# Kernel tuning notes

Hardware: AMD Instinct MI355X
Metric: run time of the kernel (lower is better)

## Reference

```python
import jax, jax.numpy as jnp
import numpy as np

B, S, D, H, DFF = 4, 2048, 1024, 16, 4096
HD = D // H  # head_dim = 64


def rmsnorm(x, scale, eps=1e-6):
    var = jnp.mean(jnp.square(x), axis=-1, keepdims=True)
    return x * jax.lax.rsqrt(var + eps) * scale


def setup_inputs() -> dict:
    key = jax.random.key(0)
    ks = jax.random.split(key, 16)
    s = 1.0 / np.sqrt(D)
    inp = {
        "x": jax.random.normal(ks[0], (B, S, D), jnp.float32),
        "wq": jax.random.normal(ks[1], (D, D), jnp.float32) * s,
        "bq": jnp.zeros((D,), jnp.float32),
        "wk": jax.random.normal(ks[2], (D, D), jnp.float32) * s,
        "bk": jnp.zeros((D,), jnp.float32),
        "wv": jax.random.normal(ks[3], (D, D), jnp.float32) * s,
        "bv": jnp.zeros((D,), jnp.float32),
        "wbeta": jax.random.normal(ks[4], (D, H), jnp.float32) * s,
        "bbeta": jnp.zeros((H,), jnp.float32),
        "wo": jax.random.normal(ks[5], (D, D), jnp.float32) * s,
        "bo": jnp.zeros((D,), jnp.float32),
        "w1": jax.random.normal(ks[6], (D, DFF), jnp.float32) * s,
        "b1": jnp.zeros((DFF,), jnp.float32),
        "w2": jax.random.normal(ks[7], (DFF, D), jnp.float32) * (1.0 / np.sqrt(DFF)),
        "b2": jnp.zeros((D,), jnp.float32),
        "ln1_scale": jnp.ones((D,), jnp.float32),
        "ln2_scale": jnp.ones((D,), jnp.float32),
    }
    return inp


def gdn_attention(x, wq, bq, wk, bk, wv, bv, wbeta, bbeta, wo, bo):
    b, s, _ = x.shape
    q = (x @ wq + bq).reshape(b, s, H, HD)
    k = (x @ wk + bk).reshape(b, s, H, HD)
    v = (x @ wv + bv).reshape(b, s, H, HD)
    k = k / (jnp.linalg.norm(k, axis=-1, keepdims=True) + 1e-6)
    beta = jax.nn.sigmoid(x @ wbeta + bbeta)[..., None]  # (b, s, H, 1)

    # time-major for scan: (s, b, H, ...)
    q = jnp.transpose(q, (1, 0, 2, 3))
    k = jnp.transpose(k, (1, 0, 2, 3))
    v = jnp.transpose(v, (1, 0, 2, 3))
    beta = jnp.transpose(beta, (1, 0, 2, 3))

    def _step(Sm, inputs):
        q_t, k_t, v_t, beta_t = inputs
        Sk = jnp.einsum('bhde,bhe->bhd', Sm, k_t)
        delta = v_t - Sk
        Sm = Sm + beta_t[..., None] * jnp.einsum('bhd,bhe->bhde', delta, k_t)
        o_t = jnp.einsum('bhde,bhe->bhd', Sm, q_t)
        return Sm, o_t

    S0 = jnp.zeros((b, H, HD, HD), x.dtype)
    _, outputs = jax.lax.scan(_step, S0, (q, k, v, beta))
    outputs = jnp.transpose(outputs, (1, 0, 2, 3)).reshape(b, s, D)
    return outputs @ wo + bo


def reference(x, wq, bq, wk, bk, wv, bv, wbeta, bbeta, wo, bo,
              w1, b1, w2, b2, ln1_scale, ln2_scale):
    residual = x
    h = rmsnorm(x, ln1_scale)
    h = gdn_attention(h, wq, bq, wk, bk, wv, bv, wbeta, bbeta, wo, bo)
    x = h + residual
    residual = x
    h = rmsnorm(x, ln2_scale)
    h = jax.nn.gelu(h @ w1 + b1) @ w2 + b2
    return h + residual
```

## Files before the change

### kernel.cpp

```cpp
#include <hip/hip_runtime.h>

#define DEV __device__ __forceinline__

typedef short bf16x8 __attribute__((ext_vector_type(8)));
typedef float f32x4 __attribute__((ext_vector_type(4)));
typedef unsigned int uint;

DEV unsigned short f2b(float f) {
    uint u = __float_as_uint(f);
    u += 0x7fffu + ((u >> 16) & 1u);
    return (unsigned short)(u >> 16);
}
DEV uint packbf2(float a, float b) { return (uint)f2b(a) | ((uint)f2b(b) << 16); }
DEV float b2f(unsigned short s) { return __uint_as_float(((uint)s) << 16); }
DEV float b2f_lo(uint u) { return __uint_as_float(u << 16); }
DEV float b2f_hi(uint u) { return __uint_as_float(u & 0xffff0000u); }

DEV void async_cp16(const void* g, void* l) {
    __builtin_amdgcn_global_load_lds(
        (const __attribute__((address_space(1))) unsigned int*)g,
        (__attribute__((address_space(3))) unsigned int*)l, 16, 0, 0);
}

DEV float quad_sum(float x) {
    x += __int_as_float(__builtin_amdgcn_update_dpp(0, __float_as_int(x), 0xB1, 0xF, 0xF, true));
    x += __int_as_float(__builtin_amdgcn_update_dpp(0, __float_as_int(x), 0x4E, 0xF, 0xF, true));
    return x;
}

DEV float gelu_f(float u) {
    float p = u + 0.044715f * u * u * u;
    float e = __expf(-1.5957691216f * p);
    return __fdividef(u, 1.f + e);
}

DEV void dec8(uint4 p, float* o) {
    o[0] = b2f_lo(p.x); o[1] = b2f_hi(p.x); o[2] = b2f_lo(p.y); o[3] = b2f_hi(p.y);
    o[4] = b2f_lo(p.z); o[5] = b2f_hi(p.z); o[6] = b2f_lo(p.w); o[7] = b2f_hi(p.w);
}

__global__ __launch_bounds__(256) void transpose_cast_k(
    const float* __restrict__ in, unsigned short* __restrict__ out, int K, int N)
{
    __shared__ float tile[32][33];
    const int k0 = blockIdx.x * 32, n0 = blockIdx.y * 32;
    const int tx = threadIdx.x & 31, ty = threadIdx.x >> 5;
#pragma unroll
    for (int i = 0; i < 32; i += 8) {
        int n = n0 + tx;
        tile[ty + i][tx] = (n < N) ? in[(size_t)(k0 + ty + i) * N + n] : 0.0f;
    }
    __syncthreads();
#pragma unroll
    for (int i = 0; i < 32; i += 8) {
        out[(size_t)(n0 + ty + i) * K + (k0 + tx)] = f2b(tile[tx][ty + i]);
    }
}

__global__ void build_bias_k(const float* __restrict__ bq, const float* __restrict__ bk,
                             const float* __restrict__ bv, const float* __restrict__ bb,
                             float* __restrict__ outb)
{
    int i = blockIdx.x * 256 + threadIdx.x;
    if (i >= 3200) return;
    float v = 0.f;
    if (i < 1024)      v = bq[i];
    else if (i < 2048) v = bk[i - 1024];
    else if (i < 3072) v = bv[i - 2048];
    else if (i < 3088) v = bb[i - 3072];
    outb[i] = v;
}

__global__ __launch_bounds__(256) void rmsnorm_cast_k(
    const float* __restrict__ x, const float* __restrict__ scale,
    unsigned short* __restrict__ out)
{
    const int row = blockIdx.x;
    const int t = threadIdx.x;
    const float4 v = *(const float4*)(x + (size_t)row * 1024 + t * 4);
    float ss = v.x * v.x + v.y * v.y + v.z * v.z + v.w * v.w;
#pragma unroll
    for (int off = 1; off < 64; off <<= 1) ss += __shfl_xor(ss, off);
    __shared__ float wsum[4];
    if ((t & 63) == 0) wsum[t >> 6] = ss;
    __syncthreads();
    const float tot = wsum[0] + wsum[1] + wsum[2] + wsum[3];
    const float inv = rsqrtf(tot * (1.0f / 1024.0f) + 1e-6f);
    const float4 sc = *(const float4*)(scale + t * 4);
    uint lo = (uint)f2b(v.x * inv * sc.x) | ((uint)f2b(v.y * inv * sc.y) << 16);
    uint hi = (uint)f2b(v.z * inv * sc.z) | ((uint)f2b(v.w * inv * sc.w) << 16);
    uint2 pkd; pkd.x = lo; pkd.y = hi;
    *(uint2*)(out + (size_t)row * 1024 + t * 4) = pkd;
}

template <int MODE>
__global__ __launch_bounds__(256) void gemm_bt(
    const unsigned short* __restrict__ A, const unsigned short* __restrict__ BT,
    const float* __restrict__ bias, const float* __restrict__ add,
    void* __restrict__ Cout, int N, int K)
{
    __shared__ unsigned short As[128 * 32];
    __shared__ unsigned short Bs[128 * 32];
    const int tid = threadIdx.x;
    const int wid = tid >> 6;
    const int lane = tid & 63;
    const int m0 = blockIdx.x * 128;
    const int n0 = blockIdx.y * 128;

    const int lrow = lane >> 2;
    const int lkw = (((lane & 3) ^ ((lane >> 3) & 3))) * 8;

    const unsigned short* Ag0 = A + (size_t)(m0 + wid * 16 + lrow) * K + lkw;
    const unsigned short* Ag1 = A + (size_t)(m0 + wid * 16 + 64 + lrow) * K + lkw;
    const unsigned short* Bg0 = BT + (size_t)(n0 + wid * 16 + lrow) * K + lkw;
    const unsigned short* Bg1 = BT + (size_t)(n0 + wid * 16 + 64 + lrow) * K + lkw;
    unsigned short* As0 = &As[(wid * 16) * 32];
    unsigned short* As1 = &As[(wid * 16 + 64) * 32];
    unsigned short* Bs0 = &Bs[(wid * 16) * 32];
    unsigned short* Bs1 = &Bs[(wid * 16 + 64) * 32];

    f32x4 acc[4][4];
#pragma unroll
    for (int i = 0; i < 4; i++)
#pragma unroll
        for (int j = 0; j < 4; j++) acc[i][j] = (f32x4)0.f;

    const int wm = (wid & 1) * 64;
    const int wn = (wid >> 1) * 64;
    const int l16 = lane & 15;
    const int quad = lane >> 4;
    const int koffs = (quad ^ ((l16 >> 1) & 3)) * 8;

    for (int k0 = 0; k0 < K; k0 += 32) {
        async_cp16(Ag0 + k0, As0);
        async_cp16(Ag1 + k0, As1);
        async_cp16(Bg0 + k0, Bs0);
        async_cp16(Bg1 + k0, Bs1);
        __syncthreads();
        bf16x8 af[4], bfv[4];
#pragma unroll
        for (int i = 0; i < 4; i++) af[i] = *(const bf16x8*)&As[(wm + i * 16 + l16) * 32 + koffs];
#pragma unroll
        for (int j = 0; j < 4; j++) bfv[j] = *(const bf16x8*)&Bs[(wn + j * 16 + l16) * 32 + koffs];
#pragma unroll
        for (int i = 0; i < 4; i++)
#pragma unroll
            for (int j = 0; j < 4; j++)
                acc[i][j] = __builtin_amdgcn_mfma_f32_16x16x32_bf16(af[i], bfv[j], acc[i][j], 0, 0, 0);
        __syncthreads();
    }

    if (MODE == 2 || MODE == 3) {
        float* ep = ((wid & 2) ? (float*)Bs : (float*)As) + (wid & 1) * 1024;
        const int rr = lane >> 2, cg = lane & 3;
        unsigned short* Cu = (unsigned short*)Cout;
#pragma unroll
        for (int i = 0; i < 4; i++) {
#pragma unroll
            for (int p = 0; p < 2; p++) {
#pragma unroll
                for (int jj = 0; jj < 2; jj++) {
                    const int j = 2 * p + jj;
                    const float bv = bias[n0 + wn + j * 16 + l16];
#pragma unroll
                    for (int r = 0; r < 4; r++) {
                        float v = acc[i][j][r] + bv;
                        if (MODE == 2) v = gelu_f(v);
                        ep[(jj * 16 + l16) * 17 + quad * 4 + r] = v;
                    }
                }
                __syncthreads();
                uint4 pk;
                float f[8];
#pragma unroll
                for (int m = 0; m < 8; m++) f[m] = ep[(cg * 8 + m) * 17 + rr];
                pk.x = packbf2(f[0], f[1]); pk.y = packbf2(f[2], f[3]);
                pk.z = packbf2(f[4], f[5]); pk.w = packbf2(f[6], f[7]);
                *(uint4*)(Cu + (size_t)(m0 + wm + i * 16 + rr) * N + (n0 + wn + p * 32 + cg * 8)) = pk;
                __syncthreads();
            }
        }
    } else {
#pragma unroll
        for (int j = 0; j < 4; j++) {
            const int cg2 = n0 + wn + j * 16 + l16;
            const float bv = bias[cg2];
#pragma unroll
            for (int i = 0; i < 4; i++) {
                const int rg0 = m0 + wm + i * 16 + quad * 4;
#pragma unroll
                for (int r = 0; r < 4; r++) {
                    size_t idx = (size_t)(rg0 + r) * N + cg2;
                    float v = acc[i][j][r] + bv;
                    if (MODE == 1) v += add[idx];
                    ((float*)Cout)[idx] = v;
                }
            }
        }
    }
}


__global__ __launch_bounds__(256) void gdn_prep(
    unsigned short* __restrict__ qkv, unsigned short* __restrict__ Wg,
    unsigned short* __restrict__ ZTg, unsigned short* __restrict__ KTg)
{
    const int chunk = blockIdx.x, bh = blockIdx.y;
    const int b = bh >> 4, h = bh & 15;
    __shared__ float Ks[64 * 68];
    __shared__ float Ws[64 * 65];
    __shared__ float Zs[64 * 65];
    __shared__ float Asl[64 * 65];
    __shared__ float bs[64];
    const int tid = threadIdx.x;
    const int t = tid >> 2, c = tid & 3;
    unsigned short* rowp = qkv + (size_t)(b * 2048 + chunk * 64 + t) * 3200;

    float kn[16];
    {
        uint4 ka = *(const uint4*)(rowp + 1024 + h * 64 + 16 * c);
        uint4 kb = *(const uint4*)(rowp + 1024 + h * 64 + 16 * c + 8);
        dec8(ka, kn); dec8(kb, kn + 8);
    }
    float ss = 0.f;
#pragma unroll
    for (int j = 0; j < 16; j++) ss += kn[j] * kn[j];
    ss = quad_sum(ss);
    const float inv = 1.f / (sqrtf(ss) + 1e-6f);
#pragma unroll
    for (int j = 0; j < 16; j++) kn[j] *= inv;
#pragma unroll
    for (int j = 0; j < 16; j++) Ks[t * 68 + 16 * c + j] = kn[j];
    {
        uint4 p0, p1;
        p0.x = packbf2(kn[0], kn[1]);  p0.y = packbf2(kn[2], kn[3]);
        p0.z = packbf2(kn[4], kn[5]);  p0.w = packbf2(kn[6], kn[7]);
        p1.x = packbf2(kn[8], kn[9]);  p1.y = packbf2(kn[10], kn[11]);
        p1.z = packbf2(kn[12], kn[13]); p1.w = packbf2(kn[14], kn[15]);
        *(uint4*)(rowp + 1024 + h * 64 + 16 * c) = p0;
        *(uint4*)(rowp + 1024 + h * 64 + 16 * c + 8) = p1;
    }
    if (c == 0) bs[t] = 1.f / (1.f + __expf(-b2f(rowp[3072 + h])));
    __syncthreads();

    const float beta = bs[t];
#pragma unroll
    for (int j = 0; j < 16; j++) Ws[t * 65 + 16 * c + j] = beta * kn[j];
    {
        float vv[16];
        uint4 va = *(const uint4*)(rowp + 2048 + h * 64 + 16 * c);
        uint4 vb = *(const uint4*)(rowp + 2048 + h * 64 + 16 * c + 8);
        dec8(va, vv); dec8(vb, vv + 8);
#pragma unroll
        for (int j = 0; j < 16; j++) Zs[t * 65 + 16 * c + j] = beta * vv[j];
    }
    __syncthreads();

    {
        const int tt = tid >> 4, sx = tid & 15;
        float dm[4][4];
#pragma unroll
        for (int i = 0; i < 4; i++)
#pragma unroll
            for (int j = 0; j < 4; j++) dm[i][j] = 0.f;
        for (int d = 0; d < 64; d++) {
            float kt[4], ksv[4];
#pragma unroll
            for (int i = 0; i < 4; i++) kt[i] = Ks[(4 * tt + i) * 68 + d];
#pragma unroll
            for (int j = 0; j < 4; j++) ksv[j] = Ks[(4 * sx + j) * 68 + d];
#pragma unroll
            for (int i = 0; i < 4; i++)
#pragma unroll
                for (int j = 0; j < 4; j++) dm[i][j] += kt[i] * ksv[j];
        }
#pragma unroll
        for (int i = 0; i < 4; i++)
#pragma unroll
            for (int j = 0; j < 4; j++) {
                int T = 4 * tt + i, S_ = 4 * sx + j;
                Asl[T * 65 + S_] = (S_ < T) ? bs[T] * dm[i][j] : 0.f;
            }
    }
    __syncthreads();

    {
        const int wid = tid >> 6, lane = tid & 63;
        for (int qi = 0; qi < 4; qi++) {
            if (qi > 0) {
                const int tb = qi * 16 + wid * 4;
                float aw[4], az[4];
#pragma unroll
                for (int i = 0; i < 4; i++) { aw[i] = Ws[(tb + i) * 65 + lane]; az[i] = Zs[(tb + i) * 65 + lane]; }
                for (int s = 0; s < qi * 16; s++) {
                    float wsv = Ws[s * 65 + lane], zsv = Zs[s * 65 + lane];
#pragma unroll
                    for (int i = 0; i < 4; i++) {
                        float a = Asl[(tb + i) * 65 + s];
                        aw[i] -= a * wsv; az[i] -= a * zsv;
                    }
                }
#pragma unroll
                for (int i = 0; i < 4; i++) { Ws[(tb + i) * 65 + lane] = aw[i]; Zs[(tb + i) * 65 + lane] = az[i]; }
            }
            __syncthreads();
            if (wid == 0) {
                for (int T = qi * 16; T < qi * 16 + 16; T++) {
                    float a_ = Ws[T * 65 + lane];
                    for (int s = qi * 16; s < T; s++) a_ -= Asl[T * 65 + s] * Ws[s * 65 + lane];
                    Ws[T * 65 + lane] = a_;
                }
            } else if (wid == 1) {
                for (int T = qi * 16; T < qi * 16 + 16; T++) {
                    float a_ = Zs[T * 65 + lane];
                    for (int s = qi * 16; s < T; s++) a_ -= Asl[T * 65 + s] * Zs[s * 65 + lane];
                    Zs[T * 65 + lane] = a_;
                }
            }
            __syncthreads();
        }
    }

    const size_t cbase = ((size_t)bh * 32 + chunk) * 4096;
    {
#pragma unroll
        for (int half = 0; half < 2; half++) {
            uint4 w4;
            w4.x = packbf2(Ws[t * 65 + 16 * c + half * 8 + 0], Ws[t * 65 + 16 * c + half * 8 + 1]);
            w4.y = packbf2(Ws[t * 65 + 16 * c + half * 8 + 2], Ws[t * 65 + 16 * c + half * 8 + 3]);
            w4.z = packbf2(Ws[t * 65 + 16 * c + half * 8 + 4], Ws[t * 65 + 16 * c + half * 8 + 5]);
            w4.w = packbf2(Ws[t * 65 + 16 * c + half * 8 + 6], Ws[t * 65 + 16 * c + half * 8 + 7]);
            *(uint4*)(Wg + cbase + (size_t)((2 * c + half) * 64 + t) * 8) = w4;
        }
    }
    {
        const int jj = tid >> 2, tq = tid & 3;
#pragma unroll
        for (int half = 0; half < 2; half++) {
            uint4 z4;
            int i0 = half * 8;
            z4.x = packbf2(Zs[(16 * tq + i0 + 0) * 65 + jj], Zs[(16 * tq + i0 + 1) * 65 + jj]);
            z4.y = packbf2(Zs[(16 * tq + i0 + 2) * 65 + jj], Zs[(16 * tq + i0 + 3) * 65 + jj]);
            z4.z = packbf2(Zs[(16 * tq + i0 + 4) * 65 + jj], Zs[(16 * tq + i0 + 5) * 65 + jj]);
            z4.w = packbf2(Zs[(16 * tq + i0 + 6) * 65 + jj], Zs[(16 * tq + i0 + 7) * 65 + jj]);
            *(uint4*)(ZTg + cbase + (size_t)((2 * tq + half) * 64 + jj) * 8) = z4;
        }
    }
    {
        const int dd = tid >> 2, tq = tid & 3;
#pragma unroll
        for (int half = 0; half < 2; half++) {
            uint4 k4;
            int i0 = half * 8;
            k4.x = packbf2(Ks[(16 * tq + i0 + 0) * 68 + dd], Ks[(16 * tq + i0 + 1) * 68 + dd]);
            k4.y = packbf2(Ks[(16 * tq + i0 + 2) * 68 + dd], Ks[(16 * tq + i0 + 3) * 68 + dd]);
            k4.z = packbf2(Ks[(16 * tq + i0 + 4) * 68 + dd], Ks[(16 * tq + i0 + 5) * 68 + dd]);
            k4.w = packbf2(Ks[(16 * tq + i0 + 6) * 68 + dd], Ks[(16 * tq + i0 + 7) * 68 + dd]);
            *(uint4*)(KTg + cbase + (size_t)((2 * tq + half) * 64 + dd) * 8) = k4;
        }
    }
}

__global__ __launch_bounds__(256, 1) void gdn_prop_mfma(
    const unsigned short* __restrict__ Wg, const unsigned short* __restrict__ KTg,
    const unsigned short* __restrict__ ZTg, unsigned short* __restrict__ Sall,
    unsigned short* __restrict__ Yg)
{
    const int bh = blockIdx.x;
    __shared__ unsigned short WbU[4096];
    __shared__ unsigned short KTbU[4096];
    __shared__ unsigned short ZTbU[4096];
    __shared__ unsigned short SbU[4096];
    const int tid = threadIdx.x;
    const int wid = tid >> 6;
    const int lane = tid & 63;
    const int l16 = lane & 15, quad = lane >> 4;

    f32x4 Sacc[4];
#pragma unroll
    for (int dt = 0; dt < 4; dt++) Sacc[dt] = (f32x4)0.f;

    for (int ch = 0; ch < 32; ch++) {
        const size_t cbase = ((size_t)bh * 32 + ch) * 4096;
#pragma unroll
        for (int p = 0; p < 2; p++) {
            const int n = wid * 2 + p;
            async_cp16(Wg + cbase + n * 512 + lane * 8, &WbU[n * 512]);
            async_cp16(KTg + cbase + n * 512 + lane * 8, &KTbU[n * 512]);
            async_cp16(ZTg + cbase + n * 512 + lane * 8, &ZTbU[n * 512]);
        }
#pragma unroll
        for (int dt = 0; dt < 4; dt++) {
#pragma unroll
            for (int r = 0; r < 4; r++) {
                const int j = wid * 16 + quad * 4 + r;
                SbU[((2 * dt + (l16 >> 3)) * 64 + j) * 8 + (l16 & 7)] = f2b(Sacc[dt][r]);
            }
            const int d = dt * 16 + l16;
            uint2 sp;
            sp.x = packbf2(Sacc[dt][0], Sacc[dt][1]);
            sp.y = packbf2(Sacc[dt][2], Sacc[dt][3]);
            *(uint2*)(Sall + cbase + d * 64 + wid * 16 + quad * 4) = sp;
        }
        __syncthreads();

        f32x4 t1[4];
#pragma unroll
        for (int tt = 0; tt < 4; tt++) t1[tt] = (f32x4)0.f;
#pragma unroll
        for (int kh = 0; kh < 2; kh++) {
            const int g = kh * 4 + quad;
            bf16x8 afr = *(const bf16x8*)&SbU[(g * 64 + wid * 16 + l16) * 8];
#pragma unroll
            for (int tt = 0; tt < 4; tt++) {
                bf16x8 bfr = *(const bf16x8*)&WbU[(g * 64 + tt * 16 + l16) * 8];
                t1[tt] = __builtin_amdgcn_mfma_f32_16x16x32_bf16(afr, bfr, t1[tt], 0, 0, 0);
            }
        }
#pragma unroll
        for (int tt = 0; tt < 4; tt++) {
            const int t = tt * 16 + l16;
            const int gb = (t >> 3) * 64;
            unsigned short ybf[4];
#pragma unroll
            for (int r = 0; r < 4; r++) {
                const int j = wid * 16 + quad * 4 + r;
                const float z = b2f(ZTbU[(gb + j) * 8 + (t & 7)]);
                ybf[r] = f2b(z - t1[tt][r]);
            }
#pragma unroll
            for (int r = 0; r < 4; r++) {
                const int j = wid * 16 + quad * 4 + r;
                ZTbU[(gb + j) * 8 + (t & 7)] = ybf[r];
            }
            uint2 yp;
            yp.x = (uint)ybf[0] | ((uint)ybf[1] << 16);
            yp.y = (uint)ybf[2] | ((uint)ybf[3] << 16);
            *(uint2*)(Yg + cbase + t * 64 + wid * 16 + quad * 4) = yp;
        }
#pragma unroll
        for (int kh = 0; kh < 2; kh++) {
            const int g = kh * 4 + quad;
            bf16x8 afr = *(const bf16x8*)&ZTbU[(g * 64 + wid * 16 + l16) * 8];
#pragma unroll
            for (int dt = 0; dt < 4; dt++) {
                bf16x8 bfr = *(const bf16x8*)&KTbU[(g * 64 + dt * 16 + l16) * 8];
                Sacc[dt] = __builtin_amdgcn_mfma_f32_16x16x32_bf16(afr, bfr, Sacc[dt], 0, 0, 0);
            }
        }
        __syncthreads();
    }
}

__global__ __launch_bounds__(256) void gdn_out(
    const unsigned short* __restrict__ qkv, const unsigned short* __restrict__ Yg,
    const unsigned short* __restrict__ Sall, unsigned short* __restrict__ attn)
{
    const int chunk = blockIdx.x, bh = blockIdx.y;
    const int b = bh >> 4, h = bh & 15;
    __shared__ float Qf[64 * 68];
    __shared__ float SfT[64 * 68];
    __shared__ float Ms[64 * 65];
    __shared__ uint Kp[64 * 33];
    __shared__ uint Yp[64 * 34];
    const int tid = threadIdx.x;
    const int t = tid >> 2, c = tid & 3;
    const size_t cbase = ((size_t)bh * 32 + chunk) * 4096;

    {
        const unsigned short* rowp = qkv + (size_t)(b * 2048 + chunk * 64 + t) * 3200;
        float qv[16];
        uint4 qa = *(const uint4*)(rowp + h * 64 + 16 * c);
        uint4 qb = *(const uint4*)(rowp + h * 64 + 16 * c + 8);
        dec8(qa, qv); dec8(qb, qv + 8);
#pragma unroll
        for (int m = 0; m < 16; m++) Qf[t * 68 + 16 * c + m] = qv[m];
        uint4 ka = *(const uint4*)(rowp + 1024 + h * 64 + 16 * c);
        uint4 kb = *(const uint4*)(rowp + 1024 + h * 64 + 16 * c + 8);
        Kp[t * 33 + 8 * c + 0] = ka.x; Kp[t * 33 + 8 * c + 1] = ka.y;
        Kp[t * 33 + 8 * c + 2] = ka.z; Kp[t * 33 + 8 * c + 3] = ka.w;
        Kp[t * 33 + 8 * c + 4] = kb.x; Kp[t * 33 + 8 * c + 5] = kb.y;
        Kp[t * 33 + 8 * c + 6] = kb.z; Kp[t * 33 + 8 * c + 7] = kb.w;
        const unsigned short* yrow = Yg + cbase + t * 64 + 16 * c;
        uint4 ya = *(const uint4*)yrow;
        uint4 yb = *(const uint4*)(yrow + 8);
        Yp[t * 34 + 8 * c + 0] = ya.x; Yp[t * 34 + 8 * c + 1] = ya.y;
        Yp[t * 34 + 8 * c + 2] = ya.z; Yp[t * 34 + 8 * c + 3] = ya.w;
        Yp[t * 34 + 8 * c + 4] = yb.x; Yp[t * 34 + 8 * c + 5] = yb.y;
        Yp[t * 34 + 8 * c + 6] = yb.z; Yp[t * 34 + 8 * c + 7] = yb.w;
        const unsigned short* srow = Sall + cbase + t * 64 + 16 * c;
        float sv[16];
        uint4 sa = *(const uint4*)srow;
        uint4 sb = *(const uint4*)(srow + 8);
        dec8(sa, sv); dec8(sb, sv + 8);
#pragma unroll
        for (int m = 0; m < 16; m++) SfT[t * 68 + 16 * c + m] = sv[m];
    }
    __syncthreads();

    const int tt = tid >> 4, sx = tid & 15;
    {
        float dm[4][4];
#pragma unroll
        for (int i = 0; i < 4; i++)
#pragma unroll
            for (int j = 0; j < 4; j++) dm[i][j] = 0.f;
        for (int p = 0; p < 32; p++) {
            float q0[4], q1[4];
#pragma unroll
            for (int i = 0; i < 4; i++) {
                q0[i] = Qf[(4 * tt + i) * 68 + 2 * p];
                q1[i] = Qf[(4 * tt + i) * 68 + 2 * p + 1];
            }
#pragma unroll
            for (int j = 0; j < 4; j++) {
                uint kp = Kp[(4 * sx + j) * 33 + p];
                float kk0 = b2f_lo(kp), kk1 = b2f_hi(kp);
#pragma unroll
                for (int i = 0; i < 4; i++) dm[i][j] += q0[i] * kk0 + q1[i] * kk1;
            }
        }
#pragma unroll
        for (int i = 0; i < 4; i++)
#pragma unroll
            for (int j = 0; j < 4; j++) {
                int T = 4 * tt + i, S_ = 4 * sx + j;
                Ms[T * 65 + S_] = (S_ <= T) ? dm[i][j] : 0.f;
            }
    }
    __syncthreads();

    {
        float o[4][4];
#pragma unroll
        for (int i = 0; i < 4; i++)
#pragma unroll
            for (int j = 0; j < 4; j++) o[i][j] = 0.f;
        for (int d = 0; d < 64; d++) {
            float qv[4];
#pragma unroll
            for (int i = 0; i < 4; i++) qv[i] = Qf[(4 * tt + i) * 68 + d];
#pragma unroll
            for (int j = 0; j < 4; j++) {
                float sv = SfT[d * 68 + 4 * sx + j];
#pragma unroll
                for (int i = 0; i < 4; i++) o[i][j] += qv[i] * sv;
            }
        }
        for (int s = 0; s < 64; s++) {
            float mv[4];
#pragma unroll
            for (int i = 0; i < 4; i++) mv[i] = Ms[(4 * tt + i) * 65 + s];
            uint2 yp2 = *(const uint2*)&Yp[s * 34 + 2 * sx];
            float yv0 = b2f_lo(yp2.x), yv1 = b2f_hi(yp2.x), yv2 = b2f_lo(yp2.y), yv3 = b2f_hi(yp2.y);
#pragma unroll
            for (int i = 0; i < 4; i++) {
                o[i][0] += mv[i] * yv0; o[i][1] += mv[i] * yv1;
                o[i][2] += mv[i] * yv2; o[i][3] += mv[i] * yv3;
            }
        }
#pragma unroll
        for (int i = 0; i < 4; i++) {
            uint2 op; op.x = packbf2(o[i][0], o[i][1]); op.y = packbf2(o[i][2], o[i][3]);
            *(uint2*)(attn + (size_t)(b * 2048 + chunk * 64 + 4 * tt + i) * 1024 + h * 64 + 4 * sx) = op;
        }
    }
}

static constexpr size_t OFF_H     = 0;
static constexpr size_t OFF_WQKVT = OFF_H + 16777216;
static constexpr size_t OFF_WOT   = OFF_WQKVT + 6553600;
static constexpr size_t OFF_W1T   = OFF_WOT + 2097152;
static constexpr size_t OFF_W2T   = OFF_W1T + 8388608;
static constexpr size_t OFF_BIAS  = OFF_W2T + 8388608;
static constexpr size_t OFF_QKV   = OFF_BIAS + 16384;
static constexpr size_t OFF_ATTN  = OFF_QKV + 67108864;
static constexpr size_t OFF_Y1    = OFF_ATTN + 16777216;
static constexpr size_t OFF_WG    = OFF_Y1 + 33554432;
static constexpr size_t OFF_YG    = OFF_WG + 16777216;

extern "C" void kernel_launch(void* const* d_in, const int* in_sizes, int n_in,
                              void* d_out, int out_size, void* d_ws, size_t ws_size,
                              hipStream_t stream)
{
    const float* x     = (const float*)d_in[0];
    const float* wq    = (const float*)d_in[1];
    const float* bq    = (const float*)d_in[2];
    const float* wk    = (const float*)d_in[3];
    const float* bk    = (const float*)d_in[4];
    const float* wv    = (const float*)d_in[5];
    const float* bv    = (const float*)d_in[6];
    const float* wbeta = (const float*)d_in[7];
    const float* bbeta = (const float*)d_in[8];
    const float* wo    = (const float*)d_in[9];
    const float* bo    = (const float*)d_in[10];
    const float* w1    = (const float*)d_in[11];
    const float* b1    = (const float*)d_in[12];
    const float* w2    = (const float*)d_in[13];
    const float* b2    = (const float*)d_in[14];
    const float* ln1   = (const float*)d_in[15];
    const float* ln2   = (const float*)d_in[16];

    char* ws = (char*)d_ws;
    unsigned short* hbuf  = (unsigned short*)(ws + OFF_H);
    unsigned short* Sall  = (unsigned short*)(ws + OFF_H);
    unsigned short* wqkvT = (unsigned short*)(ws + OFF_WQKVT);
    unsigned short* woT   = (unsigned short*)(ws + OFF_WOT);
    unsigned short* w1T   = (unsigned short*)(ws + OFF_W1T);
    unsigned short* w2T   = (unsigned short*)(ws + OFF_W2T);
    float*          biasc = (float*)(ws + OFF_BIAS);
    unsigned short* qkvU  = (unsigned short*)(ws + OFF_QKV);
    unsigned short* gbuf  = (unsigned short*)(ws + OFF_QKV);
    unsigned short* attn  = (unsigned short*)(ws + OFF_ATTN);
    float*          y1    = (float*)(ws + OFF_Y1);
    unsigned short* ZTg   = (unsigned short*)(ws + OFF_Y1);
    unsigned short* KTg   = (unsigned short*)(ws + OFF_Y1 + 16777216);
    unsigned short* Wg    = (unsigned short*)(ws + OFF_WG);
    unsigned short* Yg    = (unsigned short*)(ws + OFF_YG);
    float*          out   = (float*)d_out;

    transpose_cast_k<<<dim3(32, 32), 256, 0, stream>>>(wq, wqkvT,               1024, 1024);
    transpose_cast_k<<<dim3(32, 32), 256, 0, stream>>>(wk, wqkvT + 1024 * 1024, 1024, 1024);
    transpose_cast_k<<<dim3(32, 32), 256, 0, stream>>>(wv, wqkvT + 2048 * 1024, 1024, 1024);
    transpose_cast_k<<<dim3(32, 4),  256, 0, stream>>>(wbeta, wqkvT + 3072 * 1024, 1024, 16);
    transpose_cast_k<<<dim3(32, 32), 256, 0, stream>>>(wo, woT, 1024, 1024);
    transpose_cast_k<<<dim3(32, 128), 256, 0, stream>>>(w1, w1T, 1024, 4096);
    transpose_cast_k<<<dim3(128, 32), 256, 0, stream>>>(w2, w2T, 4096, 1024);
    build_bias_k<<<13, 256, 0, stream>>>(bq, bk, bv, bbeta, biasc);

    rmsnorm_cast_k<<<8192, 256, 0, stream>>>(x, ln1, hbuf);
    gemm_bt<3><<<dim3(64, 25), 256, 0, stream>>>(hbuf, wqkvT, biasc, nullptr, qkvU, 3200, 1024);
    gdn_prep<<<dim3(32, 64), 256, 0, stream>>>(qkvU, Wg, ZTg, KTg);
    gdn_prop_mfma<<<64, 256, 0, stream>>>(Wg, KTg, ZTg, Sall, Yg);
    gdn_out<<<dim3(32, 64), 256, 0, stream>>>(qkvU, Yg, Sall, attn);
    gemm_bt<1><<<dim3(64, 8), 256, 0, stream>>>(attn, woT, bo, x, y1, 1024, 1024);
    rmsnorm_cast_k<<<8192, 256, 0, stream>>>(y1, ln2, hbuf);
    gemm_bt<2><<<dim3(64, 32), 256, 0, stream>>>(hbuf, w1T, b1, nullptr, gbuf, 4096, 1024);
    gemm_bt<1><<<dim3(64, 8), 256, 0, stream>>>(gbuf, w2T, b2, y1, out, 1024, 4096);
}
```

Baseline: 685.7 us.

## Add 256x256 four-stage pipelined MFMA GEMM for QKV and FFN-up projections

Introduces a new 512-thread GEMM kernel with 256x256 output tiles, a four-buffer LDS ring using direct global-to-LDS loads, and interleaved loads and MFMA with priority hints. It replaces the 128x128 GEMM for the fused QKV+beta projection and the GELU FFN-up projection. The aim is to raise arithmetic intensity and hide memory latency. To make the padded QKV weight fit the larger tile, the weight buffer is moved to another workspace region and the bias and transpose ranges are extended to 3328 rows. This risks higher register pressure, lower occupancy, and possible aliasing with the reused workspace.

Measured after the change: 684.3 us. Within noise of the previous version (-0.2%).

```diff
diff --git a/kernel.cpp b/kernel.cpp
--- a/kernel.cpp
+++ b/kernel.cpp
@@ -62,7 +62,7 @@
                              float* __restrict__ outb)
 {
     int i = blockIdx.x * 256 + threadIdx.x;
-    if (i >= 3200) return;
+    if (i >= 3328) return;
     float v = 0.f;
     if (i < 1024)      v = bq[i];
     else if (i < 2048) v = bk[i - 1024];
@@ -91,6 +91,115 @@
     uint hi = (uint)f2b(v.z * inv * sc.z) | ((uint)f2b(v.w * inv * sc.w) << 16);
     uint2 pkd; pkd.x = lo; pkd.y = hi;
     *(uint2*)(out + (size_t)row * 1024 + t * 4) = pkd;
+}
+
+template <bool GELU, bool GUARD>
+__global__ __launch_bounds__(512, 2) void gemm256(
+    const unsigned short* __restrict__ A, const unsigned short* __restrict__ BT,
+    const float* __restrict__ bias, unsigned short* __restrict__ C,
+    int Nstride, int Nreal, int K)
+{
+    __shared__ __align__(16) unsigned short As[4][256 * 32];
+    __shared__ __align__(16) unsigned short Bs[4][256 * 32];
+    const int tid = threadIdx.x;
+    const int wid = tid >> 6;
+    const int lane = tid & 63;
+    const int l16 = lane & 15, quad = lane >> 4;
+    const int wm = wid & 1, wn = wid >> 1;
+    const int m0 = blockIdx.x << 8, n0 = blockIdx.y << 8;
+
+    const int srow = (wid << 5) + (lane >> 2);
+    const int scol = (lane & 3) << 3;
+    const unsigned short* Ag = A + (size_t)(m0 + srow) * K + scol;
+    const unsigned short* Bg = BT + (size_t)(n0 + srow) * K + scol;
+    const size_t rstep16 = (size_t)16 * K;
+    const int ldst = wid << 10;
+
+    f32x4 acc[8][4];
+#pragma unroll
+    for (int i = 0; i < 8; i++)
+#pragma unroll
+        for (int j = 0; j < 4; j++) acc[i][j] = (f32x4)0.f;
+
+    const int aoff = ((wm << 7) + l16) * 32 + (quad << 3);
+    const int boff = ((wn << 6) + l16) * 32 + (quad << 3);
+
+    const int nt = K >> 5;
+    async_cp16(Ag, &As[0][ldst]);
+    async_cp16(Ag + rstep16, &As[0][ldst + 512]);
+    async_cp16(Bg, &Bs[0][ldst]);
+    async_cp16(Bg + rstep16, &Bs[0][ldst + 512]);
+    async_cp16(Ag + 32, &As[1][ldst]);
+    async_cp16(Ag + 32 + rstep16, &As[1][ldst + 512]);
+    async_cp16(Bg + 32, &Bs[1][ldst]);
+    async_cp16(Bg + 32 + rstep16, &Bs[1][ldst + 512]);
+    asm volatile("s_waitcnt vmcnt(4)" ::: "memory");
+    __builtin_amdgcn_s_barrier();
+
+    for (int tb = 0; tb < nt; tb += 4) {
+#pragma unroll
+        for (int u = 0; u < 4; ++u) {
+            const int t = tb + u;
+            const int pb = (u + 2) & 3;
+            const bool st = (t + 2) < nt;
+            const size_t kpre = (size_t)(t + 2) << 5;
+            bf16x8 af[4], bfr[4];
+#pragma unroll
+            for (int mi = 0; mi < 4; mi++) af[mi] = *(const bf16x8*)&As[u][aoff + mi * 512];
+#pragma unroll
+            for (int ni = 0; ni < 4; ni++) bfr[ni] = *(const bf16x8*)&Bs[u][boff + ni * 512];
+            if (st) {
+                async_cp16(Ag + kpre, &As[pb][ldst]);
+                async_cp16(Ag + kpre + rstep16, &As[pb][ldst + 512]);
+            }
+            __builtin_amdgcn_s_barrier();
+            asm volatile("s_waitcnt lgkmcnt(0)" ::: "memory");
+            __builtin_amdgcn_s_setprio(1);
+#pragma unroll
+            for (int mi = 0; mi < 4; mi++)
+#pragma unroll
+                for (int ni = 0; ni < 4; ni++)
+                    acc[mi][ni] = __builtin_amdgcn_mfma_f32_16x16x32_bf16(af[mi], bfr[ni], acc[mi][ni], 0, 0, 0);
+            __builtin_amdgcn_s_setprio(0);
+            __builtin_amdgcn_s_barrier();
+#pragma unroll
+            for (int mi = 0; mi < 4; mi++) af[mi] = *(const bf16x8*)&As[u][aoff + (mi + 4) * 512];
+            if (st) {
+                async_cp16(Bg + kpre, &Bs[pb][ldst]);
+                async_cp16(Bg + kpre + rstep16, &Bs[pb][ldst + 512]);
+            }
+            asm volatile("s_waitcnt vmcnt(4)" ::: "memory");
+            __builtin_amdgcn_s_barrier();
+            asm volatile("s_waitcnt lgkmcnt(0)" ::: "memory");
+            __builtin_amdgcn_s_setprio(1);
+#pragma unroll
+            for (int mi = 0; mi < 4; mi++)
+#pragma unroll
+                for (int ni = 0; ni < 4; ni++)
+                    acc[mi + 4][ni] = __builtin_amdgcn_mfma_f32_16x16x32_bf16(af[mi], bfr[ni], acc[mi + 4][ni], 0, 0, 0);
+            __builtin_amdgcn_s_setprio(0);
+            __builtin_amdgcn_s_barrier();
+        }
+    }
+
+    float bv[4];
+    const int ccol = n0 + (wn << 6) + l16;
+#pragma unroll
+    for (int ni = 0; ni < 4; ni++) bv[ni] = bias[ccol + ni * 16];
+#pragma unroll
+    for (int mi = 0; mi < 8; mi++) {
+        const int row = m0 + (wm << 7) + mi * 16 + (quad << 2);
+#pragma unroll
+        for (int r = 0; r < 4; r++) {
+            unsigned short* Crow = C + (size_t)(row + r) * Nstride + ccol;
+#pragma unroll
+            for (int ni = 0; ni < 4; ni++) {
+                float v = acc[mi][ni][r] + bv[ni];
+                if (GELU) v = gelu_f(v);
+                if (!GUARD || (ccol + ni * 16) < Nreal) Crow[ni * 16] = f2b(v);
+            }
+        }
+    }
 }
 
 template <int MODE>
@@ -604,7 +713,7 @@
     char* ws = (char*)d_ws;
     unsigned short* hbuf  = (unsigned short*)(ws + OFF_H);
     unsigned short* Sall  = (unsigned short*)(ws + OFF_H);
-    unsigned short* wqkvT = (unsigned short*)(ws + OFF_WQKVT);
+    unsigned short* wqkvT = (unsigned short*)(ws + OFF_WG);
     unsigned short* woT   = (unsigned short*)(ws + OFF_WOT);
     unsigned short* w1T   = (unsigned short*)(ws + OFF_W1T);
     unsigned short* w2T   = (unsigned short*)(ws + OFF_W2T);
@@ -622,19 +731,19 @@
     transpose_cast_k<<<dim3(32, 32), 256, 0, stream>>>(wq, wqkvT,               1024, 1024);
     transpose_cast_k<<<dim3(32, 32), 256, 0, stream>>>(wk, wqkvT + 1024 * 1024, 1024, 1024);
     transpose_cast_k<<<dim3(32, 32), 256, 0, stream>>>(wv, wqkvT + 2048 * 1024, 1024, 1024);
-    transpose_cast_k<<<dim3(32, 4),  256, 0, stream>>>(wbeta, wqkvT + 3072 * 1024, 1024, 16);
+    transpose_cast_k<<<dim3(32, 8),  256, 0, stream>>>(wbeta, wqkvT + 3072 * 1024, 1024, 16);
     transpose_cast_k<<<dim3(32, 32), 256, 0, stream>>>(wo, woT, 1024, 1024);
     transpose_cast_k<<<dim3(32, 128), 256, 0, stream>>>(w1, w1T, 1024, 4096);
     transpose_cast_k<<<dim3(128, 32), 256, 0, stream>>>(w2, w2T, 4096, 1024);
     build_bias_k<<<13, 256, 0, stream>>>(bq, bk, bv, bbeta, biasc);
 
     rmsnorm_cast_k<<<8192, 256, 0, stream>>>(x, ln1, hbuf);
-    gemm_bt<3><<<dim3(64, 25), 256, 0, stream>>>(hbuf, wqkvT, biasc, nullptr, qkvU, 3200, 1024);
+    gemm256<false, true><<<dim3(32, 13), 512, 0, stream>>>(hbuf, wqkvT, biasc, qkvU, 3200, 3200, 1024);
     gdn_prep<<<dim3(32, 64), 256, 0, stream>>>(qkvU, Wg, ZTg, KTg);
     gdn_prop_mfma<<<64, 256, 0, stream>>>(Wg, KTg, ZTg, Sall, Yg);
     gdn_out<<<dim3(32, 64), 256, 0, stream>>>(qkvU, Yg, Sall, attn);
     gemm_bt<1><<<dim3(64, 8), 256, 0, stream>>>(attn, woT, bo, x, y1, 1024, 1024);
     rmsnorm_cast_k<<<8192, 256, 0, stream>>>(y1, ln2, hbuf);
-    gemm_bt<2><<<dim3(64, 32), 256, 0, stream>>>(hbuf, w1T, b1, nullptr, gbuf, 4096, 1024);
+    gemm256<true, false><<<dim3(32, 16), 512, 0, stream>>>(hbuf, w1T, b1, gbuf, 4096, 4096, 1024);
     gemm_bt<1><<<dim3(64, 8), 256, 0, stream>>>(gbuf, w2T, b2, y1, out, 1024, 4096);
 }
```
